# Performance work log

Hardware: AMD Instinct MI355X
Metric: run time of the kernel (lower is better)

Reference implementation:

```python
import jax, jax.numpy as jnp
import numpy as np

N = 20000   # genes
E = 200000  # global edges
P = 300     # pathways
EP = 2000   # edges per pathway (global node indices)
D = 3       # in_dim == number of omics (forced by nn.Linear(3,1))


def setup_inputs():
    key = jax.random.key(0)
    ks = jax.random.split(key, 20)
    f = lambda i, shape: jax.random.normal(ks[i], shape, dtype=jnp.float32) * 0.1
    return {
        "x": f(0, (N, D)),
        "edge_index": jax.random.randint(ks[1], (2, E), 0, N),
        "path_edges": jax.random.randint(ks[2], (P, 2, EP), 0, N),
        "W_pool": f(3, (D, D)), "b_pool": f(4, (D,)),
        "W_self": f(5, (D, D)), "W_neigh": f(6, (D, D)), "b_conv": f(7, (D,)),
        "sub_Wl": f(8, (P, D, D)), "sub_bl": f(9, (P, D)), "sub_Wr": f(10, (P, D, D)),
        "pool_Wrel": f(11, (P, D, 1)), "pool_Wroot": f(12, (P, D, 1)), "pool_b": f(13, (P, 1)),
        "gate_W": f(14, (P, D, 1)), "gate_b": f(15, (P, 1)),
        "lin_W": f(16, (D, 1)), "lin_b": f(17, (1,)),
        "mlp_W": f(18, (P, 1)), "mlp_b": f(19, (1,)),
    }


def reference(x, edge_index, path_edges, W_pool, b_pool, W_self, W_neigh, b_conv,
              sub_Wl, sub_bl, sub_Wr, pool_Wrel, pool_Wroot, pool_b,
              gate_W, gate_b, lin_W, lin_b, mlp_W, mlp_b):
    n = x.shape[0]
    # add_self_loops on the global edge_index
    loops = jnp.arange(n)
    src = jnp.concatenate([edge_index[0], loops])
    dst = jnp.concatenate([edge_index[1], loops])

    # global SAGEConv with 'pool' aggregator: max_j relu(W_pool h_j), then self + neigh
    hp = jax.nn.relu(x @ W_pool + b_pool)                       # [N,D]
    agg = jax.ops.segment_max(hp[src], dst, num_segments=n)     # [N,D] (self-loops -> no empty segments)
    h = jnp.tanh(x @ W_self + agg @ W_neigh + b_conv)           # [N,D]

    k = int(np.ceil(0.8 * n))  # SAGPooling ratio=0.8 over all N nodes (full x is passed per pathway)

    def per_path(pe, Wl, bl, Wr, Wrel, Wroot, pb, gW, gb):
        s, d = pe[0], pe[1]
        # SAGEConv (mean aggr) on pathway subgraph edges over full node set
        msum = jax.ops.segment_sum(h[s], d, num_segments=n)
        cnt = jax.ops.segment_sum(jnp.ones(s.shape, h.dtype), d, num_segments=n)
        mean = msum / jnp.maximum(cnt, 1.0)[:, None]
        xc = jax.nn.relu(mean @ Wl + bl + h @ Wr)               # [N,D]
        # SAGPooling score via GraphConv (add aggr): W_rel * sum_j x_j + W_root * x + b
        asum = jax.ops.segment_sum(xc[s], d, num_segments=n)
        score = (asum @ Wrel + xc @ Wroot + pb)[:, 0]           # [N]
        topv, perm = jax.lax.top_k(score, k)
        xk = xc[perm] * jnp.tanh(topv)[:, None]                 # [k,D]
        # GlobalAttention readout: softmax gate over kept nodes
        gate = jax.nn.softmax((xk @ gW + gb)[:, 0])             # [k]
        return jax.nn.relu(gate @ xk)                            # [D]

    readout = jax.vmap(per_path)(path_edges, sub_Wl, sub_bl, sub_Wr,
                                 pool_Wrel, pool_Wroot, pool_b, gate_W, gate_b)  # [P,D]
    r = jax.nn.relu(readout @ lin_W + lin_b).T                  # [1,P]
    # mlp: Dropout (identity in eval) -> ReLU -> Linear(P,1) -> Sigmoid
    return jax.nn.sigmoid(jax.nn.relu(r) @ mlp_W + mlp_b)       # [1,1]
```

## Files before the change

### kernel.cpp

```cpp
#include <hip/hip_runtime.h>
#include <math.h>

#define MAXM 2048
#define BMW  640
#define BS   512
#define NB   2048

__device__ __forceinline__ unsigned fkey(float f){
  unsigned u = __float_as_uint(f);
  return (u & 0x80000000u) ? ~u : (u | 0x80000000u);
}
__device__ __forceinline__ int lbin(float sc, float lo, float scl){
  int b = (int)((sc - lo) * scl);
  return b < 0 ? 0 : (b > NB-1 ? NB-1 : b);
}
__device__ __forceinline__ void hp_eval(const float* __restrict__ x, int i,
                                        const float* __restrict__ Wp,
                                        const float* __restrict__ bp, float* o){
  float x0 = x[i*3+0], x1 = x[i*3+1], x2 = x[i*3+2];
  #pragma unroll
  for (int j = 0; j < 3; ++j)
    o[j] = fmaxf(x0*Wp[0*3+j] + x1*Wp[1*3+j] + x2*Wp[2*3+j] + bp[j], 0.f);
}

__global__ void k_edge(const float* __restrict__ x, const int* __restrict__ ei,
                       const float* __restrict__ Wp, const float* __restrict__ bp,
                       float* __restrict__ agg, float* __restrict__ acc,
                       unsigned* __restrict__ counter, int E){
  if (blockIdx.x == 0 && threadIdx.x == 0){ acc[0] = 0.f; counter[0] = 0u; }
  int e = blockIdx.x*blockDim.x + threadIdx.x;
  if (e >= E) return;
  int s = ei[e], d = ei[E+e];
  float o[3]; hp_eval(x, s, Wp, bp, o);
  #pragma unroll
  for (int j = 0; j < 3; ++j)
    atomicMax((int*)&agg[d*3+j], __float_as_int(o[j]));
}

__global__ void k_h2(const float* __restrict__ x, float* __restrict__ hb,
                     const float* __restrict__ Wp, const float* __restrict__ bp,
                     const float* __restrict__ Ws, const float* __restrict__ Wn,
                     const float* __restrict__ bc, int N){
  int i = blockIdx.x*blockDim.x + threadIdx.x;
  if (i >= N) return;
  float hp[3]; hp_eval(x, i, Wp, bp, hp);
  float x0 = x[i*3+0], x1 = x[i*3+1], x2 = x[i*3+2];
  float a0 = fmaxf(hb[i*3+0], hp[0]);
  float a1 = fmaxf(hb[i*3+1], hp[1]);
  float a2 = fmaxf(hb[i*3+2], hp[2]);
  float o[3];
  #pragma unroll
  for (int j = 0; j < 3; ++j){
    float v = x0*Ws[0*3+j] + x1*Ws[1*3+j] + x2*Ws[2*3+j]
            + a0*Wn[0*3+j] + a1*Wn[1*3+j] + a2*Wn[2*3+j] + bc[j];
    o[j] = tanhf(v);
  }
  hb[i*3+0] = o[0]; hb[i*3+1] = o[1]; hb[i*3+2] = o[2];
}

__device__ __forceinline__ void pick_bucket(const unsigned* hist, int l,
    unsigned pref, unsigned mask, int shift,
    unsigned* sel_prefix, unsigned* sel_mask, int* sel_r){
  unsigned h0 = hist[4*l+0], h1 = hist[4*l+1], h2 = hist[4*l+2], h3 = hist[4*l+3];
  unsigned s = h0+h1+h2+h3;
  unsigned S = s;
  #pragma unroll
  for (int off = 1; off < 64; off <<= 1){
    unsigned t = __shfl_down(S, off);
    if (l + off < 64) S += t;
  }
  unsigned Snext = S - s;
  unsigned r = (unsigned)*sel_r;
  unsigned suf3 = h3 + Snext;
  unsigned suf2 = h2 + suf3;
  unsigned suf1 = h1 + suf2;
  unsigned suf0 = h0 + suf1;
  int b = -1; unsigned sufnext = 0;
  if      (suf3 >= r && Snext < r){ b = 4*l+3; sufnext = Snext; }
  else if (suf2 >= r && suf3  < r){ b = 4*l+2; sufnext = suf3; }
  else if (suf1 >= r && suf2  < r){ b = 4*l+1; sufnext = suf2; }
  else if (suf0 >= r && suf1  < r){ b = 4*l+0; sufnext = suf1; }
  if (b >= 0){
    *sel_prefix = pref | ((unsigned)b << shift);
    *sel_mask   = mask | (255u << shift);
    *sel_r      = (int)(r - sufnext);
  }
}

__global__ void __launch_bounds__(BS)
k_mega(const float* __restrict__ h, const int* __restrict__ pe,
       const float* __restrict__ sWl, const float* __restrict__ sbl, const float* __restrict__ sWr,
       const float* __restrict__ pWrel, const float* __restrict__ pWroot, const float* __restrict__ pB,
       const float* __restrict__ gW, const float* __restrict__ gB,
       const float* __restrict__ linW, const float* __restrict__ linb,
       const float* __restrict__ mlpW, const float* __restrict__ mlpb,
       float* __restrict__ spG, float* __restrict__ acc, unsigned* __restrict__ counter,
       unsigned* __restrict__ out, int N, int EP, int K, int P){
  __shared__ unsigned bm[BMW];
  __shared__ int      wpfx[BMW];
  __shared__ float    msum[MAXM*3];
  __shared__ unsigned scrA[NB];
  __shared__ unsigned scrB[NB];
  __shared__ float    wredf[(BS/64)*4];
  __shared__ float    s_mn, s_mx;
  __shared__ float    rlo[3], rsc[3];
  __shared__ int      rb[3];
  __shared__ int      s_r, s_C, s_cc, s_done;
  __shared__ unsigned s_uT;
  __shared__ unsigned sel_prefix, sel_mask;
  __shared__ int      sel_r;

  const int p = blockIdx.x;
  const int tid = threadIdx.x;

  float Wl[9], Wr[9], bl[3], wrel[3], wroot[3], gw[3];
  #pragma unroll
  for (int j = 0; j < 9; ++j){ Wl[j] = sWl[p*9+j]; Wr[j] = sWr[p*9+j]; }
  #pragma unroll
  for (int j = 0; j < 3; ++j){
    bl[j] = sbl[p*3+j]; wrel[j] = pWrel[p*3+j];
    wroot[j] = pWroot[p*3+j]; gw[j] = gW[p*3+j];
  }
  float pbv = pB[p], gbv = gB[p];
  float* sp = spG + (size_t)p*N;

  int*   cnt  = (int*)scrA;
  float* adot = (float*)scrB;

  for (int s = tid; s < MAXM; s += BS){
    cnt[s] = 0; adot[s] = 0.f;
    msum[s*3+0]=0.f; msum[s*3+1]=0.f; msum[s*3+2]=0.f;
  }
  for (int s = tid; s < BMW; s += BS) bm[s] = 0u;
  if (tid == 0){ s_done = 0; s_uT = 0u; }
  __syncthreads();

  const int* ps = pe + (size_t)p*2*EP;
  const int* pd = ps + EP;

  for (int e = tid; e < EP; e += BS) atomicOr(&bm[pd[e]>>5], 1u << (pd[e]&31));
  __syncthreads();
  if (tid < 64){
    int l = tid, base = l*10;
    int c[10], s = 0;
    #pragma unroll
    for (int q = 0; q < 10; ++q){ c[q] = __popc(bm[base+q]); s += c[q]; }
    int pre = s;
    #pragma unroll
    for (int off = 1; off < 64; off <<= 1){
      int t = __shfl_up(pre, off);
      if (l >= off) pre += t;
    }
    pre -= s;
    #pragma unroll
    for (int q = 0; q < 10; ++q){ wpfx[base+q] = pre; pre += c[q]; }
  }
  __syncthreads();
  for (int e = tid; e < EP; e += BS){
    int s = ps[e], d = pd[e];
    int r = wpfx[d>>5] + __popc(bm[d>>5] & ((1u << (d&31)) - 1u));
    atomicAdd(&cnt[r], 1);
    atomicAdd(&msum[r*3+0], h[s*3+0]);
    atomicAdd(&msum[r*3+1], h[s*3+1]);
    atomicAdd(&msum[r*3+2], h[s*3+2]);
  }
  __syncthreads();
  for (int r = tid; r < MAXM; r += BS){
    int c = cnt[r];
    if (c > 0){
      float inv = 1.f / (float)c;
      msum[r*3+0] *= inv; msum[r*3+1] *= inv; msum[r*3+2] *= inv;
    }
  }
  __syncthreads();
  for (int e = tid; e < EP; e += BS){
    int s = ps[e], d = pd[e];
    float m0=0.f,m1=0.f,m2=0.f;
    unsigned w = bm[s>>5];
    if ((w >> (s&31)) & 1u){
      int rs = wpfx[s>>5] + __popc(w & ((1u << (s&31)) - 1u));
      m0 = msum[rs*3+0]; m1 = msum[rs*3+1]; m2 = msum[rs*3+2];
    }
    float h0 = h[s*3+0], h1 = h[s*3+1], h2 = h[s*3+2];
    float x0 = fmaxf(m0*Wl[0]+m1*Wl[3]+m2*Wl[6] + bl[0] + h0*Wr[0]+h1*Wr[3]+h2*Wr[6], 0.f);
    float x1 = fmaxf(m0*Wl[1]+m1*Wl[4]+m2*Wl[7] + bl[1] + h0*Wr[1]+h1*Wr[4]+h2*Wr[7], 0.f);
    float x2 = fmaxf(m0*Wl[2]+m1*Wl[5]+m2*Wl[8] + bl[2] + h0*Wr[2]+h1*Wr[5]+h2*Wr[8], 0.f);
    int rd = wpfx[d>>5] + __popc(bm[d>>5] & ((1u << (d&31)) - 1u));
    atomicAdd(&adot[rd], x0*wrel[0] + x1*wrel[1] + x2*wrel[2]);
  }
  __syncthreads();

  float mn = 3.0e38f, mx = -3.0e38f;
  for (int i = tid; i < N; i += BS){
    float m0=0.f,m1=0.f,m2=0.f,ad=0.f;
    unsigned w = bm[i>>5];
    if ((w >> (i&31)) & 1u){
      int r = wpfx[i>>5] + __popc(w & ((1u << (i&31)) - 1u));
      m0 = msum[r*3+0]; m1 = msum[r*3+1]; m2 = msum[r*3+2];
      ad = adot[r];
    }
    float h0 = h[i*3+0], h1 = h[i*3+1], h2 = h[i*3+2];
    float x0 = fmaxf(m0*Wl[0]+m1*Wl[3]+m2*Wl[6] + bl[0] + h0*Wr[0]+h1*Wr[3]+h2*Wr[6], 0.f);
    float x1 = fmaxf(m0*Wl[1]+m1*Wl[4]+m2*Wl[7] + bl[1] + h0*Wr[1]+h1*Wr[4]+h2*Wr[7], 0.f);
    float x2 = fmaxf(m0*Wl[2]+m1*Wl[5]+m2*Wl[8] + bl[2] + h0*Wr[2]+h1*Wr[5]+h2*Wr[8], 0.f);
    float sc = ad + x0*wroot[0]+x1*wroot[1]+x2*wroot[2] + pbv;
    sp[i] = sc;
    mn = fminf(mn, sc); mx = fmaxf(mx, sc);
  }
  #pragma unroll
  for (int off = 32; off > 0; off >>= 1){
    mn = fminf(mn, __shfl_down(mn, off));
    mx = fmaxf(mx, __shfl_down(mx, off));
  }
  if ((tid & 63) == 0){ int w = tid>>6; wredf[w*2+0] = mn; wredf[w*2+1] = mx; }
  __syncthreads();
  if (tid == 0){
    float a = 3.0e38f, b = -3.0e38f;
    for (int w = 0; w < BS/64; ++w){ a = fminf(a, wredf[w*2+0]); b = fmaxf(b, wredf[w*2+1]); }
    s_mn = a; s_mx = b; s_r = K;
    if (!(b > a)){ s_uT = fkey(a); s_done = 1; }
  }
  __syncthreads();

  unsigned* hist = scrA;
  unsigned* cand = scrB;

  for (int t = 0; t < 3; ++t){
    __syncthreads();
    if (s_done) break;
    float lo, hi;
    if (t == 0){ lo = s_mn; hi = s_mx; }
    else { lo = rlo[t-1] + rb[t-1]/rsc[t-1]; hi = rlo[t-1] + (rb[t-1]+1)/rsc[t-1]; }
    float scl = 2047.0f / (hi - lo);
    if (!(hi > lo) || !(scl < 1e37f)){
      if (tid == 0){ s_uT = fkey(lo); s_done = 1; }
      __syncthreads();
      continue;
    }
    for (int b = tid; b < NB; b += BS) hist[b] = 0u;
    __syncthreads();
    if (t == 0){
      if ((N & 3) == 0){
        int G = N >> 2;
        for (int g = tid; g < G; g += BS){
          float4 v = ((const float4*)sp)[g];
          atomicAdd(&hist[lbin(v.x, lo, scl)], 1u);
          atomicAdd(&hist[lbin(v.y, lo, scl)], 1u);
          atomicAdd(&hist[lbin(v.z, lo, scl)], 1u);
          atomicAdd(&hist[lbin(v.w, lo, scl)], 1u);
        }
      } else {
        for (int i = tid; i < N; i += BS) atomicAdd(&hist[lbin(sp[i], lo, scl)], 1u);
      }
    } else {
      for (int i = tid; i < N; i += BS){
        float sc = sp[i];
        bool act = true;
        for (int q = 0; q < t; ++q) act = act && (lbin(sc, rlo[q], rsc[q]) == rb[q]);
        if (act) atomicAdd(&hist[lbin(sc, lo, scl)], 1u);
      }
    }
    __syncthreads();
    if (tid < 64){
      int l = tid;
      unsigned cs[32]; unsigned s = 0;
      #pragma unroll
      for (int q = 0; q < 32; ++q){ cs[q] = hist[l*32+q]; s += cs[q]; }
      unsigned S = s;
      #pragma unroll
      for (int off = 1; off < 64; off <<= 1){
        unsigned u2 = __shfl_down(S, off);
        if (l + off < 64) S += u2;
      }
      unsigned suf = S - s;
      unsigned r = (unsigned)s_r;
      int b = -1; unsigned sufnext = 0, cb = 0;
      for (int q = 31; q >= 0; --q){
        unsigned nsuf = suf + cs[q];
        if (nsuf >= r && suf < r){ b = l*32+q; sufnext = suf; cb = cs[q]; }
        suf = nsuf;
      }
      if (b >= 0){
        rb[t] = b; rlo[t] = lo; rsc[t] = scl;
        s_r = (int)(r - sufnext);
        s_C = (int)cb;
      }
    }
    __syncthreads();
    int C = s_C;
    if (C <= NB){
      if (tid == 0) s_cc = 0;
      __syncthreads();
      for (int i = tid; i < N; i += BS){
        float sc = sp[i];
        bool act = true;
        for (int q = 0; q <= t; ++q) act = act && (lbin(sc, rlo[q], rsc[q]) == rb[q]);
        if (act){ int ix = atomicAdd(&s_cc, 1); if (ix < NB) cand[ix] = fkey(sc); }
      }
      __syncthreads();
      if (tid == 0){ sel_prefix = 0u; sel_mask = 0u; sel_r = s_r; }
      __syncthreads();
      for (int pass = 0; pass < 4; ++pass){
        int shift = 24 - 8*pass;
        if (tid < 256) hist[tid] = 0u;
        __syncthreads();
        unsigned mask = sel_mask, pref = sel_prefix;
        for (int j = tid; j < C; j += BS){
          unsigned u = cand[j];
          if ((u & mask) == pref) atomicAdd(&hist[(u>>shift)&255u], 1u);
        }
        __syncthreads();
        if (tid < 64)
          pick_bucket(hist, tid, pref, mask, shift, &sel_prefix, &sel_mask, &sel_r);
        __syncthreads();
      }
      if (tid == 0){ s_uT = sel_prefix; s_done = 1; }
      __syncthreads();
    } else if (t == 2){
      if (tid == 0){ s_uT = fkey(lo + rb[t]/scl); s_done = 1; }
      __syncthreads();
    }
  }
  __syncthreads();
  const unsigned uT = s_uT;

  float l = 0.f, a0 = 0.f, a1 = 0.f, a2 = 0.f;
  for (int i = tid; i < N; i += BS){
    float sc = sp[i];
    if (fkey(sc) >= uT){
      float m0=0.f,m1=0.f,m2=0.f;
      unsigned w = bm[i>>5];
      if ((w >> (i&31)) & 1u){
        int r = wpfx[i>>5] + __popc(w & ((1u << (i&31)) - 1u));
        m0 = msum[r*3+0]; m1 = msum[r*3+1]; m2 = msum[r*3+2];
      }
      float h0 = h[i*3+0], h1 = h[i*3+1], h2 = h[i*3+2];
      float x0 = fmaxf(m0*Wl[0]+m1*Wl[3]+m2*Wl[6] + bl[0] + h0*Wr[0]+h1*Wr[3]+h2*Wr[6], 0.f);
      float x1 = fmaxf(m0*Wl[1]+m1*Wl[4]+m2*Wl[7] + bl[1] + h0*Wr[1]+h1*Wr[4]+h2*Wr[7], 0.f);
      float x2 = fmaxf(m0*Wl[2]+m1*Wl[5]+m2*Wl[8] + bl[2] + h0*Wr[2]+h1*Wr[5]+h2*Wr[8], 0.f);
      float tt = tanhf(sc);
      x0 *= tt; x1 *= tt; x2 *= tt;
      float g = x0*gw[0] + x1*gw[1] + x2*gw[2] + gbv;
      g = fminf(fmaxf(g, -60.f), 60.f);
      float e = expf(g);
      l += e; a0 += e*x0; a1 += e*x1; a2 += e*x2;
    }
  }
  #pragma unroll
  for (int off = 32; off > 0; off >>= 1){
    l  += __shfl_down(l,  off);
    a0 += __shfl_down(a0, off);
    a1 += __shfl_down(a1, off);
    a2 += __shfl_down(a2, off);
  }
  if ((tid & 63) == 0){
    int w = tid >> 6;
    wredf[w*4+0]=l; wredf[w*4+1]=a0; wredf[w*4+2]=a1; wredf[w*4+3]=a2;
  }
  __syncthreads();
  if (tid == 0){
    float L=0.f, A0=0.f, A1=0.f, A2=0.f;
    for (int w = 0; w < BS/64; ++w){
      L += wredf[w*4+0]; A0 += wredf[w*4+1]; A1 += wredf[w*4+2]; A2 += wredf[w*4+3];
    }
    float inv = 1.f / L;
    float r0 = fmaxf(A0*inv, 0.f);
    float r1 = fmaxf(A1*inv, 0.f);
    float r2 = fmaxf(A2*inv, 0.f);
    float rr = fmaxf(r0*linW[0] + r1*linW[1] + r2*linW[2] + linb[0], 0.f);
    atomicAdd(acc, rr * mlpW[p]);
    __threadfence();
    unsigned old = atomicAdd(counter, 1u);
    if (old == (unsigned)(P-1)){
      __threadfence();
      float z = atomicAdd(acc, 0.f) + mlpb[0];
      float a = 1.f / (1.f + expf(-z));
      unsigned A = __float_as_uint(a);
      unsigned B = (A + 0x7FFFu + ((A >> 16) & 1u)) >> 16;
      out[0] = (A & 0xFFFF0000u) | (B & 0xFFFFu);
    }
  }
}

extern "C" void kernel_launch(void* const* d_in, const int* in_sizes, int n_in,
                              void* d_out, int out_size, void* d_ws, size_t ws_size,
                              hipStream_t stream){
  const float* x      = (const float*)d_in[0];
  const int*   ei     = (const int*)  d_in[1];
  const int*   pe     = (const int*)  d_in[2];
  const float* W_pool = (const float*)d_in[3];
  const float* b_pool = (const float*)d_in[4];
  const float* W_self = (const float*)d_in[5];
  const float* W_neigh= (const float*)d_in[6];
  const float* b_conv = (const float*)d_in[7];
  const float* sWl    = (const float*)d_in[8];
  const float* sbl    = (const float*)d_in[9];
  const float* sWr    = (const float*)d_in[10];
  const float* pWrel  = (const float*)d_in[11];
  const float* pWroot = (const float*)d_in[12];
  const float* pB     = (const float*)d_in[13];
  const float* gW     = (const float*)d_in[14];
  const float* gB     = (const float*)d_in[15];
  const float* linW   = (const float*)d_in[16];
  const float* linb   = (const float*)d_in[17];
  const float* mlpW   = (const float*)d_in[18];
  const float* mlpb   = (const float*)d_in[19];

  const int N  = in_sizes[0] / 3;
  const int E  = in_sizes[1] / 2;
  const int P  = in_sizes[13];
  const int EP = in_sizes[2] / (2 * P);
  const int K  = (4*N + 4) / 5;

  float*    ws      = (float*)d_ws;
  float*    acc     = ws;
  unsigned* counter = (unsigned*)(ws + 1);
  float*    agg     = ws + 16;
  float*    h       = agg;
  float*    spG     = ws + 16 + (size_t)3*N;

  k_edge<<<(E+255)/256, 256, 0, stream>>>(x, ei, W_pool, b_pool, agg, acc, counter, E);
  k_h2  <<<(N+255)/256, 256, 0, stream>>>(x, agg, W_pool, b_pool,
                                          W_self, W_neigh, b_conv, N);
  k_mega<<<P, BS, 0, stream>>>(h, pe, sWl, sbl, sWr, pWrel, pWroot, pB, gW, gB,
                               linW, linb, mlpW, mlpb,
                               spG, acc, counter, (unsigned*)d_out, N, EP, K, P);
}
```

Before: 275.9 us.

## Split per-pathway mega kernel into agg, score, select, and readout kernels

Replaces the single block-per-pathway megakernel with four stages. Edge aggregation runs per pathway, score computation and readout are spread over 10 chunks per pathway, and top-k threshold selection uses 1024-thread blocks. The intent is to raise GPU occupancy: 300 blocks of 512 threads underfill the device, and the node-wide loops over 20000 nodes dominate. In exchange, per-pathway mean/adot/bitmap state goes through global memory, there are extra launches, and the final reduction now uses per-pathway partial atomics plus a last-block combine.

```diff
diff --git a/kernel.cpp b/kernel.cpp
--- a/kernel.cpp
+++ b/kernel.cpp
@@ -3,8 +3,8 @@
 
 #define MAXM 2048
 #define BMW  640
-#define BS   512
 #define NB   2048
+#define SELBS 1024
 
 __device__ __forceinline__ unsigned fkey(float f){
   unsigned u = __float_as_uint(f);
@@ -25,9 +25,8 @@
 
 __global__ void k_edge(const float* __restrict__ x, const int* __restrict__ ei,
                        const float* __restrict__ Wp, const float* __restrict__ bp,
-                       float* __restrict__ agg, float* __restrict__ acc,
-                       unsigned* __restrict__ counter, int E){
-  if (blockIdx.x == 0 && threadIdx.x == 0){ acc[0] = 0.f; counter[0] = 0u; }
+                       float* __restrict__ agg, unsigned* __restrict__ counter, int E){
+  if (blockIdx.x == 0 && threadIdx.x == 0) counter[0] = 0u;
   int e = blockIdx.x*blockDim.x + threadIdx.x;
   if (e >= E) return;
   int s = ei[e], d = ei[E+e];
@@ -56,6 +55,169 @@
     o[j] = tanhf(v);
   }
   hb[i*3+0] = o[0]; hb[i*3+1] = o[1]; hb[i*3+2] = o[2];
+}
+
+__global__ void __launch_bounds__(512)
+k_agg(const float* __restrict__ h, const int* __restrict__ pe,
+      const float* __restrict__ sWl, const float* __restrict__ sbl, const float* __restrict__ sWr,
+      const float* __restrict__ pWrel,
+      unsigned* __restrict__ bmG, int* __restrict__ wpfxG,
+      float* __restrict__ meanG, float* __restrict__ adotG,
+      float* __restrict__ part, int EP){
+  __shared__ unsigned bm[BMW];
+  __shared__ int      wpfx[BMW];
+  __shared__ float    msum[MAXM*3];
+  __shared__ int      cnt[MAXM];
+  __shared__ float    adot[MAXM];
+
+  const int p = blockIdx.x;
+  const int tid = threadIdx.x;
+
+  if (tid < 4) part[p*4 + tid] = 0.f;
+
+  float Wl[9], Wr[9], bl[3], wrel[3];
+  #pragma unroll
+  for (int j = 0; j < 9; ++j){ Wl[j] = sWl[p*9+j]; Wr[j] = sWr[p*9+j]; }
+  #pragma unroll
+  for (int j = 0; j < 3; ++j){ bl[j] = sbl[p*3+j]; wrel[j] = pWrel[p*3+j]; }
+
+  for (int s = tid; s < MAXM; s += 512){
+    cnt[s] = 0; adot[s] = 0.f;
+    msum[s*3+0]=0.f; msum[s*3+1]=0.f; msum[s*3+2]=0.f;
+  }
+  for (int s = tid; s < BMW; s += 512) bm[s] = 0u;
+  __syncthreads();
+
+  const int* ps = pe + (size_t)p*2*EP;
+  const int* pd = ps + EP;
+
+  for (int e = tid; e < EP; e += 512) atomicOr(&bm[pd[e]>>5], 1u << (pd[e]&31));
+  __syncthreads();
+
+  if (tid < 64){
+    int l = tid, base = l*10;
+    int c[10], s = 0;
+    #pragma unroll
+    for (int q = 0; q < 10; ++q){ c[q] = __popc(bm[base+q]); s += c[q]; }
+    int pre = s;
+    #pragma unroll
+    for (int off = 1; off < 64; off <<= 1){
+      int t = __shfl_up(pre, off);
+      if (l >= off) pre += t;
+    }
+    pre -= s;
+    #pragma unroll
+    for (int q = 0; q < 10; ++q){ wpfx[base+q] = pre; pre += c[q]; }
+  }
+  __syncthreads();
+
+  for (int e = tid; e < EP; e += 512){
+    int s = ps[e], d = pd[e];
+    int r = wpfx[d>>5] + __popc(bm[d>>5] & ((1u << (d&31)) - 1u));
+    atomicAdd(&cnt[r], 1);
+    atomicAdd(&msum[r*3+0], h[s*3+0]);
+    atomicAdd(&msum[r*3+1], h[s*3+1]);
+    atomicAdd(&msum[r*3+2], h[s*3+2]);
+  }
+  __syncthreads();
+
+  for (int r = tid; r < MAXM; r += 512){
+    int c = cnt[r];
+    if (c > 0){
+      float inv = 1.f / (float)c;
+      msum[r*3+0] *= inv; msum[r*3+1] *= inv; msum[r*3+2] *= inv;
+    }
+  }
+  __syncthreads();
+
+  for (int e = tid; e < EP; e += 512){
+    int s = ps[e], d = pd[e];
+    float m0=0.f,m1=0.f,m2=0.f;
+    unsigned w = bm[s>>5];
+    if ((w >> (s&31)) & 1u){
+      int rs = wpfx[s>>5] + __popc(w & ((1u << (s&31)) - 1u));
+      m0 = msum[rs*3+0]; m1 = msum[rs*3+1]; m2 = msum[rs*3+2];
+    }
+    float h0 = h[s*3+0], h1 = h[s*3+1], h2 = h[s*3+2];
+    float x0 = fmaxf(m0*Wl[0]+m1*Wl[3]+m2*Wl[6] + bl[0] + h0*Wr[0]+h1*Wr[3]+h2*Wr[6], 0.f);
+    float x1 = fmaxf(m0*Wl[1]+m1*Wl[4]+m2*Wl[7] + bl[1] + h0*Wr[1]+h1*Wr[4]+h2*Wr[7], 0.f);
+    float x2 = fmaxf(m0*Wl[2]+m1*Wl[5]+m2*Wl[8] + bl[2] + h0*Wr[2]+h1*Wr[5]+h2*Wr[8], 0.f);
+    int rd = wpfx[d>>5] + __popc(bm[d>>5] & ((1u << (d&31)) - 1u));
+    atomicAdd(&adot[rd], x0*wrel[0] + x1*wrel[1] + x2*wrel[2]);
+  }
+  __syncthreads();
+
+  for (int q = tid; q < MAXM*3; q += 512) meanG[(size_t)p*MAXM*3 + q] = msum[q];
+  for (int q = tid; q < MAXM;   q += 512) adotG[(size_t)p*MAXM + q]   = adot[q];
+  for (int q = tid; q < BMW;    q += 512){ bmG[(size_t)p*BMW + q] = bm[q]; wpfxG[(size_t)p*BMW + q] = wpfx[q]; }
+}
+
+__device__ __forceinline__ void node_eval_g(int i, const float* __restrict__ h,
+    const unsigned* __restrict__ bmP, const int* __restrict__ wpfxP,
+    const float* __restrict__ meanP, const float* __restrict__ adotP,
+    const float* Wl, const float* bl, const float* Wr,
+    const float* wroot, float pbv,
+    float& sc, float* xc){
+  float m0=0.f,m1=0.f,m2=0.f,ad=0.f;
+  unsigned w = bmP[i>>5];
+  if ((w >> (i&31)) & 1u){
+    int r = wpfxP[i>>5] + __popc(w & ((1u << (i&31)) - 1u));
+    m0 = meanP[r*3+0]; m1 = meanP[r*3+1]; m2 = meanP[r*3+2];
+    ad = adotP[r];
+  }
+  float h0 = h[i*3+0], h1 = h[i*3+1], h2 = h[i*3+2];
+  xc[0] = fmaxf(m0*Wl[0]+m1*Wl[3]+m2*Wl[6] + bl[0] + h0*Wr[0]+h1*Wr[3]+h2*Wr[6], 0.f);
+  xc[1] = fmaxf(m0*Wl[1]+m1*Wl[4]+m2*Wl[7] + bl[1] + h0*Wr[1]+h1*Wr[4]+h2*Wr[7], 0.f);
+  xc[2] = fmaxf(m0*Wl[2]+m1*Wl[5]+m2*Wl[8] + bl[2] + h0*Wr[2]+h1*Wr[5]+h2*Wr[8], 0.f);
+  sc = ad + xc[0]*wroot[0]+xc[1]*wroot[1]+xc[2]*wroot[2] + pbv;
+}
+
+__device__ __forceinline__ void xc_eval_g(int i, const float* __restrict__ h,
+    const unsigned* __restrict__ bmP, const int* __restrict__ wpfxP,
+    const float* __restrict__ meanP,
+    const float* Wl, const float* bl, const float* Wr, float* xc){
+  float m0=0.f,m1=0.f,m2=0.f;
+  unsigned w = bmP[i>>5];
+  if ((w >> (i&31)) & 1u){
+    int r = wpfxP[i>>5] + __popc(w & ((1u << (i&31)) - 1u));
+    m0 = meanP[r*3+0]; m1 = meanP[r*3+1]; m2 = meanP[r*3+2];
+  }
+  float h0 = h[i*3+0], h1 = h[i*3+1], h2 = h[i*3+2];
+  xc[0] = fmaxf(m0*Wl[0]+m1*Wl[3]+m2*Wl[6] + bl[0] + h0*Wr[0]+h1*Wr[3]+h2*Wr[6], 0.f);
+  xc[1] = fmaxf(m0*Wl[1]+m1*Wl[4]+m2*Wl[7] + bl[1] + h0*Wr[1]+h1*Wr[4]+h2*Wr[7], 0.f);
+  xc[2] = fmaxf(m0*Wl[2]+m1*Wl[5]+m2*Wl[8] + bl[2] + h0*Wr[2]+h1*Wr[5]+h2*Wr[8], 0.f);
+}
+
+__global__ void __launch_bounds__(256)
+k_score(const float* __restrict__ h,
+        const float* __restrict__ sWl, const float* __restrict__ sbl, const float* __restrict__ sWr,
+        const float* __restrict__ pWroot, const float* __restrict__ pB,
+        const unsigned* __restrict__ bmG, const int* __restrict__ wpfxG,
+        const float* __restrict__ meanG, const float* __restrict__ adotG,
+        float* __restrict__ scoreG, int N, int SCH, int CH){
+  const int bx = blockIdx.x;
+  const int p = bx / SCH, c = bx % SCH;
+  const int tid = threadIdx.x;
+  const int start = c*CH, end = min(start + CH, N);
+
+  float Wl[9], Wr[9], bl[3], wroot[3];
+  #pragma unroll
+  for (int j = 0; j < 9; ++j){ Wl[j] = sWl[p*9+j]; Wr[j] = sWr[p*9+j]; }
+  #pragma unroll
+  for (int j = 0; j < 3; ++j){ bl[j] = sbl[p*3+j]; wroot[j] = pWroot[p*3+j]; }
+  float pbv = pB[p];
+
+  const unsigned* bmP  = bmG  + (size_t)p*BMW;
+  const int*     wpfxP = wpfxG+ (size_t)p*BMW;
+  const float*   meanP = meanG+ (size_t)p*MAXM*3;
+  const float*   adotP = adotG+ (size_t)p*MAXM;
+  float*         sp    = scoreG + (size_t)p*N;
+
+  for (int i = start + tid; i < end; i += 256){
+    float sc, xcv[3];
+    node_eval_g(i, h, bmP, wpfxP, meanP, adotP, Wl, bl, Wr, wroot, pbv, sc, xcv);
+    sp[i] = sc;
+  }
 }
 
 __device__ __forceinline__ void pick_bucket(const unsigned* hist, int l,
@@ -87,21 +249,11 @@
   }
 }
 
-__global__ void __launch_bounds__(BS)
-k_mega(const float* __restrict__ h, const int* __restrict__ pe,
-       const float* __restrict__ sWl, const float* __restrict__ sbl, const float* __restrict__ sWr,
-       const float* __restrict__ pWrel, const float* __restrict__ pWroot, const float* __restrict__ pB,
-       const float* __restrict__ gW, const float* __restrict__ gB,
-       const float* __restrict__ linW, const float* __restrict__ linb,
-       const float* __restrict__ mlpW, const float* __restrict__ mlpb,
-       float* __restrict__ spG, float* __restrict__ acc, unsigned* __restrict__ counter,
-       unsigned* __restrict__ out, int N, int EP, int K, int P){
-  __shared__ unsigned bm[BMW];
-  __shared__ int      wpfx[BMW];
-  __shared__ float    msum[MAXM*3];
-  __shared__ unsigned scrA[NB];
-  __shared__ unsigned scrB[NB];
-  __shared__ float    wredf[(BS/64)*4];
+__global__ void __launch_bounds__(SELBS)
+k_sel(const float* __restrict__ scoreG, unsigned* __restrict__ uTG, int N, int K){
+  __shared__ unsigned hist[NB];
+  __shared__ unsigned cand[NB];
+  __shared__ float    wredf[(SELBS/64)*2];
   __shared__ float    s_mn, s_mx;
   __shared__ float    rlo[3], rsc[3];
   __shared__ int      rb[3];
@@ -112,100 +264,19 @@
 
   const int p = blockIdx.x;
   const int tid = threadIdx.x;
-
-  float Wl[9], Wr[9], bl[3], wrel[3], wroot[3], gw[3];
-  #pragma unroll
-  for (int j = 0; j < 9; ++j){ Wl[j] = sWl[p*9+j]; Wr[j] = sWr[p*9+j]; }
-  #pragma unroll
-  for (int j = 0; j < 3; ++j){
-    bl[j] = sbl[p*3+j]; wrel[j] = pWrel[p*3+j];
-    wroot[j] = pWroot[p*3+j]; gw[j] = gW[p*3+j];
-  }
-  float pbv = pB[p], gbv = gB[p];
-  float* sp = spG + (size_t)p*N;
-
-  int*   cnt  = (int*)scrA;
-  float* adot = (float*)scrB;
-
-  for (int s = tid; s < MAXM; s += BS){
-    cnt[s] = 0; adot[s] = 0.f;
-    msum[s*3+0]=0.f; msum[s*3+1]=0.f; msum[s*3+2]=0.f;
-  }
-  for (int s = tid; s < BMW; s += BS) bm[s] = 0u;
+  const float* sp = scoreG + (size_t)p*N;
+
   if (tid == 0){ s_done = 0; s_uT = 0u; }
-  __syncthreads();
-
-  const int* ps = pe + (size_t)p*2*EP;
-  const int* pd = ps + EP;
-
-  for (int e = tid; e < EP; e += BS) atomicOr(&bm[pd[e]>>5], 1u << (pd[e]&31));
-  __syncthreads();
-  if (tid < 64){
-    int l = tid, base = l*10;
-    int c[10], s = 0;
-    #pragma unroll
-    for (int q = 0; q < 10; ++q){ c[q] = __popc(bm[base+q]); s += c[q]; }
-    int pre = s;
-    #pragma unroll
-    for (int off = 1; off < 64; off <<= 1){
-      int t = __shfl_up(pre, off);
-      if (l >= off) pre += t;
-    }
-    pre -= s;
-    #pragma unroll
-    for (int q = 0; q < 10; ++q){ wpfx[base+q] = pre; pre += c[q]; }
-  }
-  __syncthreads();
-  for (int e = tid; e < EP; e += BS){
-    int s = ps[e], d = pd[e];
-    int r = wpfx[d>>5] + __popc(bm[d>>5] & ((1u << (d&31)) - 1u));
-    atomicAdd(&cnt[r], 1);
-    atomicAdd(&msum[r*3+0], h[s*3+0]);
-    atomicAdd(&msum[r*3+1], h[s*3+1]);
-    atomicAdd(&msum[r*3+2], h[s*3+2]);
-  }
-  __syncthreads();
-  for (int r = tid; r < MAXM; r += BS){
-    int c = cnt[r];
-    if (c > 0){
-      float inv = 1.f / (float)c;
-      msum[r*3+0] *= inv; msum[r*3+1] *= inv; msum[r*3+2] *= inv;
-    }
-  }
-  __syncthreads();
-  for (int e = tid; e < EP; e += BS){
-    int s = ps[e], d = pd[e];
-    float m0=0.f,m1=0.f,m2=0.f;
-    unsigned w = bm[s>>5];
-    if ((w >> (s&31)) & 1u){
-      int rs = wpfx[s>>5] + __popc(w & ((1u << (s&31)) - 1u));
-      m0 = msum[rs*3+0]; m1 = msum[rs*3+1]; m2 = msum[rs*3+2];
-    }
-    float h0 = h[s*3+0], h1 = h[s*3+1], h2 = h[s*3+2];
-    float x0 = fmaxf(m0*Wl[0]+m1*Wl[3]+m2*Wl[6] + bl[0] + h0*Wr[0]+h1*Wr[3]+h2*Wr[6], 0.f);
-    float x1 = fmaxf(m0*Wl[1]+m1*Wl[4]+m2*Wl[7] + bl[1] + h0*Wr[1]+h1*Wr[4]+h2*Wr[7], 0.f);
-    float x2 = fmaxf(m0*Wl[2]+m1*Wl[5]+m2*Wl[8] + bl[2] + h0*Wr[2]+h1*Wr[5]+h2*Wr[8], 0.f);
-    int rd = wpfx[d>>5] + __popc(bm[d>>5] & ((1u << (d&31)) - 1u));
-    atomicAdd(&adot[rd], x0*wrel[0] + x1*wrel[1] + x2*wrel[2]);
-  }
-  __syncthreads();
 
   float mn = 3.0e38f, mx = -3.0e38f;
-  for (int i = tid; i < N; i += BS){
-    float m0=0.f,m1=0.f,m2=0.f,ad=0.f;
-    unsigned w = bm[i>>5];
-    if ((w >> (i&31)) & 1u){
-      int r = wpfx[i>>5] + __popc(w & ((1u << (i&31)) - 1u));
-      m0 = msum[r*3+0]; m1 = msum[r*3+1]; m2 = msum[r*3+2];
-      ad = adot[r];
-    }
-    float h0 = h[i*3+0], h1 = h[i*3+1], h2 = h[i*3+2];
-    float x0 = fmaxf(m0*Wl[0]+m1*Wl[3]+m2*Wl[6] + bl[0] + h0*Wr[0]+h1*Wr[3]+h2*Wr[6], 0.f);
-    float x1 = fmaxf(m0*Wl[1]+m1*Wl[4]+m2*Wl[7] + bl[1] + h0*Wr[1]+h1*Wr[4]+h2*Wr[7], 0.f);
-    float x2 = fmaxf(m0*Wl[2]+m1*Wl[5]+m2*Wl[8] + bl[2] + h0*Wr[2]+h1*Wr[5]+h2*Wr[8], 0.f);
-    float sc = ad + x0*wroot[0]+x1*wroot[1]+x2*wroot[2] + pbv;
-    sp[i] = sc;
-    mn = fminf(mn, sc); mx = fmaxf(mx, sc);
+  int G4 = N >> 2;
+  for (int g = tid; g < G4; g += SELBS){
+    float4 v = ((const float4*)sp)[g];
+    mn = fminf(mn, fminf(fminf(v.x, v.y), fminf(v.z, v.w)));
+    mx = fmaxf(mx, fmaxf(fmaxf(v.x, v.y), fmaxf(v.z, v.w)));
+  }
+  for (int i = (G4<<2) + tid; i < N; i += SELBS){
+    float s = sp[i]; mn = fminf(mn, s); mx = fmaxf(mx, s);
   }
   #pragma unroll
   for (int off = 32; off > 0; off >>= 1){
@@ -216,14 +287,11 @@
   __syncthreads();
   if (tid == 0){
     float a = 3.0e38f, b = -3.0e38f;
-    for (int w = 0; w < BS/64; ++w){ a = fminf(a, wredf[w*2+0]); b = fmaxf(b, wredf[w*2+1]); }
+    for (int w = 0; w < SELBS/64; ++w){ a = fminf(a, wredf[w*2+0]); b = fmaxf(b, wredf[w*2+1]); }
     s_mn = a; s_mx = b; s_r = K;
     if (!(b > a)){ s_uT = fkey(a); s_done = 1; }
   }
   __syncthreads();
-
-  unsigned* hist = scrA;
-  unsigned* cand = scrB;
 
   for (int t = 0; t < 3; ++t){
     __syncthreads();
@@ -237,23 +305,20 @@
       __syncthreads();
       continue;
     }
-    for (int b = tid; b < NB; b += BS) hist[b] = 0u;
+    for (int b = tid; b < NB; b += SELBS) hist[b] = 0u;
     __syncthreads();
     if (t == 0){
-      if ((N & 3) == 0){
-        int G = N >> 2;
-        for (int g = tid; g < G; g += BS){
-          float4 v = ((const float4*)sp)[g];
-          atomicAdd(&hist[lbin(v.x, lo, scl)], 1u);
-          atomicAdd(&hist[lbin(v.y, lo, scl)], 1u);
-          atomicAdd(&hist[lbin(v.z, lo, scl)], 1u);
-          atomicAdd(&hist[lbin(v.w, lo, scl)], 1u);
-        }
-      } else {
-        for (int i = tid; i < N; i += BS) atomicAdd(&hist[lbin(sp[i], lo, scl)], 1u);
-      }
+      for (int g = tid; g < G4; g += SELBS){
+        float4 v = ((const float4*)sp)[g];
+        atomicAdd(&hist[lbin(v.x, lo, scl)], 1u);
+        atomicAdd(&hist[lbin(v.y, lo, scl)], 1u);
+        atomicAdd(&hist[lbin(v.z, lo, scl)], 1u);
+        atomicAdd(&hist[lbin(v.w, lo, scl)], 1u);
+      }
+      for (int i = (G4<<2) + tid; i < N; i += SELBS)
+        atomicAdd(&hist[lbin(sp[i], lo, scl)], 1u);
     } else {
-      for (int i = tid; i < N; i += BS){
+      for (int i = tid; i < N; i += SELBS){
         float sc = sp[i];
         bool act = true;
         for (int q = 0; q < t; ++q) act = act && (lbin(sc, rlo[q], rsc[q]) == rb[q]);
@@ -291,7 +356,7 @@
     if (C <= NB){
       if (tid == 0) s_cc = 0;
       __syncthreads();
-      for (int i = tid; i < N; i += BS){
+      for (int i = tid; i < N; i += SELBS){
         float sc = sp[i];
         bool act = true;
         for (int q = 0; q <= t; ++q) act = act && (lbin(sc, rlo[q], rsc[q]) == rb[q]);
@@ -305,7 +370,7 @@
         if (tid < 256) hist[tid] = 0u;
         __syncthreads();
         unsigned mask = sel_mask, pref = sel_prefix;
-        for (int j = tid; j < C; j += BS){
+        for (int j = tid; j < C; j += SELBS){
           unsigned u = cand[j];
           if ((u & mask) == pref) atomicAdd(&hist[(u>>shift)&255u], 1u);
         }
@@ -322,24 +387,50 @@
     }
   }
   __syncthreads();
-  const unsigned uT = s_uT;
+  if (tid == 0) uTG[p] = s_uT;
+}
+
+__global__ void __launch_bounds__(256)
+k_read(const float* __restrict__ h,
+       const float* __restrict__ sWl, const float* __restrict__ sbl, const float* __restrict__ sWr,
+       const float* __restrict__ gW, const float* __restrict__ gB,
+       const unsigned* __restrict__ bmG, const int* __restrict__ wpfxG,
+       const float* __restrict__ meanG,
+       const float* __restrict__ scoreG, const unsigned* __restrict__ uTG,
+       const float* __restrict__ linW, const float* __restrict__ linb,
+       const float* __restrict__ mlpW, const float* __restrict__ mlpb,
+       float* __restrict__ part, unsigned* __restrict__ counter,
+       unsigned* __restrict__ out, int N, int SCH, int CH, int P){
+  __shared__ float wred[4*4];
+  __shared__ int   lastflag;
+  __shared__ float sred[256];
+
+  const int bx = blockIdx.x;
+  const int p = bx / SCH, c = bx % SCH;
+  const int tid = threadIdx.x;
+  const int start = c*CH, end = min(start + CH, N);
+
+  float Wl[9], Wr[9], bl[3], gw[3];
+  #pragma unroll
+  for (int j = 0; j < 9; ++j){ Wl[j] = sWl[p*9+j]; Wr[j] = sWr[p*9+j]; }
+  #pragma unroll
+  for (int j = 0; j < 3; ++j){ bl[j] = sbl[p*3+j]; gw[j] = gW[p*3+j]; }
+  float gbv = gB[p];
+  unsigned uT = uTG[p];
+
+  const unsigned* bmP  = bmG  + (size_t)p*BMW;
+  const int*     wpfxP = wpfxG+ (size_t)p*BMW;
+  const float*   meanP = meanG+ (size_t)p*MAXM*3;
+  const float*   sp    = scoreG + (size_t)p*N;
 
   float l = 0.f, a0 = 0.f, a1 = 0.f, a2 = 0.f;
-  for (int i = tid; i < N; i += BS){
+  for (int i = start + tid; i < end; i += 256){
     float sc = sp[i];
     if (fkey(sc) >= uT){
-      float m0=0.f,m1=0.f,m2=0.f;
-      unsigned w = bm[i>>5];
-      if ((w >> (i&31)) & 1u){
-        int r = wpfx[i>>5] + __popc(w & ((1u << (i&31)) - 1u));
-        m0 = msum[r*3+0]; m1 = msum[r*3+1]; m2 = msum[r*3+2];
-      }
-      float h0 = h[i*3+0], h1 = h[i*3+1], h2 = h[i*3+2];
-      float x0 = fmaxf(m0*Wl[0]+m1*Wl[3]+m2*Wl[6] + bl[0] + h0*Wr[0]+h1*Wr[3]+h2*Wr[6], 0.f);
-      float x1 = fmaxf(m0*Wl[1]+m1*Wl[4]+m2*Wl[7] + bl[1] + h0*Wr[1]+h1*Wr[4]+h2*Wr[7], 0.f);
-      float x2 = fmaxf(m0*Wl[2]+m1*Wl[5]+m2*Wl[8] + bl[2] + h0*Wr[2]+h1*Wr[5]+h2*Wr[8], 0.f);
-      float tt = tanhf(sc);
-      x0 *= tt; x1 *= tt; x2 *= tt;
+      float xcv[3];
+      xc_eval_g(i, h, bmP, wpfxP, meanP, Wl, bl, Wr, xcv);
+      float t = tanhf(sc);
+      float x0 = xcv[0]*t, x1 = xcv[1]*t, x2 = xcv[2]*t;
       float g = x0*gw[0] + x1*gw[1] + x2*gw[2] + gbv;
       g = fminf(fmaxf(g, -60.f), 60.f);
       float e = expf(g);
@@ -355,25 +446,44 @@
   }
   if ((tid & 63) == 0){
     int w = tid >> 6;
-    wredf[w*4+0]=l; wredf[w*4+1]=a0; wredf[w*4+2]=a1; wredf[w*4+3]=a2;
+    wred[w*4+0]=l; wred[w*4+1]=a0; wred[w*4+2]=a1; wred[w*4+3]=a2;
   }
   __syncthreads();
   if (tid == 0){
     float L=0.f, A0=0.f, A1=0.f, A2=0.f;
-    for (int w = 0; w < BS/64; ++w){
-      L += wredf[w*4+0]; A0 += wredf[w*4+1]; A1 += wredf[w*4+2]; A2 += wredf[w*4+3];
-    }
-    float inv = 1.f / L;
-    float r0 = fmaxf(A0*inv, 0.f);
-    float r1 = fmaxf(A1*inv, 0.f);
-    float r2 = fmaxf(A2*inv, 0.f);
-    float rr = fmaxf(r0*linW[0] + r1*linW[1] + r2*linW[2] + linb[0], 0.f);
-    atomicAdd(acc, rr * mlpW[p]);
+    for (int w = 0; w < 4; ++w){
+      L += wred[w*4+0]; A0 += wred[w*4+1]; A1 += wred[w*4+2]; A2 += wred[w*4+3];
+    }
+    atomicAdd(&part[p*4+0], L);
+    atomicAdd(&part[p*4+1], A0);
+    atomicAdd(&part[p*4+2], A1);
+    atomicAdd(&part[p*4+3], A2);
     __threadfence();
     unsigned old = atomicAdd(counter, 1u);
-    if (old == (unsigned)(P-1)){
-      __threadfence();
-      float z = atomicAdd(acc, 0.f) + mlpb[0];
+    lastflag = (old == (unsigned)(gridDim.x - 1)) ? 1 : 0;
+  }
+  __syncthreads();
+  if (lastflag){
+    float lw0 = linW[0], lw1 = linW[1], lw2 = linW[2], lb = linb[0];
+    float v = 0.f;
+    for (int q = tid; q < P; q += 256){
+      float L  = atomicAdd(&part[q*4+0], 0.f);
+      float A0 = atomicAdd(&part[q*4+1], 0.f);
+      float A1 = atomicAdd(&part[q*4+2], 0.f);
+      float A2 = atomicAdd(&part[q*4+3], 0.f);
+      float inv = 1.f / L;
+      float r0 = fmaxf(A0*inv, 0.f);
+      float r1 = fmaxf(A1*inv, 0.f);
+      float r2 = fmaxf(A2*inv, 0.f);
+      v += fmaxf(r0*lw0 + r1*lw1 + r2*lw2 + lb, 0.f) * mlpW[q];
+    }
+    sred[tid] = v;
+    for (int s = 128; s > 0; s >>= 1){
+      __syncthreads();
+      if (tid < s) sred[tid] += sred[tid+s];
+    }
+    if (tid == 0){
+      float z = sred[0] + mlpb[0];
       float a = 1.f / (1.f + expf(-z));
       unsigned A = __float_as_uint(a);
       unsigned B = (A + 0x7FFFu + ((A >> 16) & 1u)) >> 16;
@@ -412,17 +522,41 @@
   const int EP = in_sizes[2] / (2 * P);
   const int K  = (4*N + 4) / 5;
 
-  float*    ws      = (float*)d_ws;
-  float*    acc     = ws;
-  unsigned* counter = (unsigned*)(ws + 1);
-  float*    agg     = ws + 16;
+  const size_t o_cnt  = 1;
+  const size_t o_agg  = 16;
+  const size_t o_part = o_agg  + (size_t)3*N;
+  const size_t o_uT   = o_part + (size_t)P*4;
+  const size_t o_bm   = o_uT   + (size_t)P;
+  const size_t o_wp   = o_bm   + (size_t)P*BMW;
+  const size_t o_mean = o_wp   + (size_t)P*BMW;
+  const size_t o_adot = o_mean + (size_t)P*MAXM*3;
+  const size_t o_sp   = o_adot + (size_t)P*MAXM;
+
+  float* ws = (float*)d_ws;
+  unsigned* counter = (unsigned*)(ws + o_cnt);
+  float*    agg     = ws + o_agg;
   float*    h       = agg;
-  float*    spG     = ws + 16 + (size_t)3*N;
-
-  k_edge<<<(E+255)/256, 256, 0, stream>>>(x, ei, W_pool, b_pool, agg, acc, counter, E);
-  k_h2  <<<(N+255)/256, 256, 0, stream>>>(x, agg, W_pool, b_pool,
-                                          W_self, W_neigh, b_conv, N);
-  k_mega<<<P, BS, 0, stream>>>(h, pe, sWl, sbl, sWr, pWrel, pWroot, pB, gW, gB,
-                               linW, linb, mlpW, mlpb,
-                               spG, acc, counter, (unsigned*)d_out, N, EP, K, P);
-}
+  float*    part    = ws + o_part;
+  unsigned* uTG     = (unsigned*)(ws + o_uT);
+  unsigned* bmG     = (unsigned*)(ws + o_bm);
+  int*      wpfxG   = (int*)     (ws + o_wp);
+  float*    meanG   = ws + o_mean;
+  float*    adotG   = ws + o_adot;
+  float*    spG     = ws + o_sp;
+
+  const int SCH = 10;
+  const int CH  = (N + SCH - 1) / SCH;
+
+  k_edge <<<(E+255)/256, 256, 0, stream>>>(x, ei, W_pool, b_pool, agg, counter, E);
+  k_h2   <<<(N+255)/256, 256, 0, stream>>>(x, agg, W_pool, b_pool,
+                                           W_self, W_neigh, b_conv, N);
+  k_agg  <<<P, 512, 0, stream>>>(h, pe, sWl, sbl, sWr, pWrel,
+                                 bmG, wpfxG, meanG, adotG, part, EP);
+  k_score<<<P*SCH, 256, 0, stream>>>(h, sWl, sbl, sWr, pWroot, pB,
+                                     bmG, wpfxG, meanG, adotG, spG, N, SCH, CH);
+  k_sel  <<<P, SELBS, 0, stream>>>(spG, uTG, N, K);
+  k_read <<<P*SCH, 256, 0, stream>>>(h, sWl, sbl, sWr, gW, gB,
+                                     bmG, wpfxG, meanG, spG, uTG,
+                                     linW, linb, mlpW, mlpb,
+                                     part, counter, (unsigned*)d_out, N, SCH, CH, P);
+}
```

Result: slower. 331.4 us (+20.1%).
